# Performance work log

Hardware: AMD Instinct MI355X
Metric: run time of the kernel (lower is better)

Reference implementation:

```python
import jax, jax.numpy as jnp
import numpy as np

N_NODES = 100000
N_EDGES = 1600000
IN_F, HID_F, OUT_F = 128, 128, 128


def setup_inputs() -> dict:
    key = jax.random.key(0)
    ks = jax.random.split(key, 12)
    x = jax.random.normal(ks[0], (N_NODES, IN_F), dtype=jnp.float32)
    src = jax.random.randint(ks[1], (N_EDGES,), 0, N_NODES)
    dst = jax.random.randint(ks[2], (N_EDGES,), 0, N_NODES)
    s = 1.0 / np.sqrt(IN_F)
    W1_self = jax.random.uniform(ks[3], (HID_F, IN_F), minval=-s, maxval=s)
    W1_neigh = jax.random.uniform(ks[4], (HID_F, IN_F), minval=-s, maxval=s)
    b1 = jnp.zeros((HID_F,), jnp.float32)
    s2 = 1.0 / np.sqrt(HID_F)
    W2_self = jax.random.uniform(ks[5], (OUT_F, HID_F), minval=-s2, maxval=s2)
    W2_neigh = jax.random.uniform(ks[6], (OUT_F, HID_F), minval=-s2, maxval=s2)
    b2 = jnp.zeros((OUT_F,), jnp.float32)
    s3 = 1.0 / np.sqrt(OUT_F)
    W3 = jax.random.uniform(ks[7], (OUT_F, OUT_F), minval=-s3, maxval=s3)
    b3 = jax.random.uniform(ks[8], (OUT_F,), minval=-s3, maxval=s3)
    return {"x": x, "src": src, "dst": dst,
            "W1_self": W1_self, "W1_neigh": W1_neigh, "b1": b1,
            "W2_self": W2_self, "W2_neigh": W2_neigh, "b2": b2,
            "W3": W3, "b3": b3}


def _sage_conv(h, src, dst, W_self, W_neigh, b):
    # DGL SAGEConv 'mean': h_neigh = mean over in-neighbors (src -> dst)
    msg = h[src]  # [E, d] irregular gather
    summed = jax.ops.segment_sum(msg, dst, num_segments=N_NODES)  # [N, d]
    deg = jax.ops.segment_sum(jnp.ones((src.shape[0],), h.dtype), dst,
                              num_segments=N_NODES)
    h_neigh = summed / jnp.clip(deg, 1.0)[:, None]
    return h @ W_self.T + h_neigh @ W_neigh.T + b


def reference(x, src, dst, W1_self, W1_neigh, b1, W2_self, W2_neigh, b2, W3, b3):
    h = _sage_conv(x, src, dst, W1_self, W1_neigh, b1)
    h = jax.nn.relu(h)
    h = _sage_conv(h, src, dst, W2_self, W2_neigh, b2)
    return h @ W3.T + b3
```

## Files before the change

kernel.cpp:

```cpp
#include <hip/hip_runtime.h>

#define N_NODES 100000
#define N_EDGES 1600000
#define F 128
#define NB_SCAN ((N_NODES + 1023) / 1024)
#define NSUB 32
#define SUB_NODES (N_NODES / NSUB)
#define BCAP 128
#define PCAP 65536
#define NCVT ((N_NODES * F / 8 + 255) / 256)

typedef short short8 __attribute__((ext_vector_type(8)));
typedef float f32x4 __attribute__((ext_vector_type(4)));
typedef unsigned short ushort_t;
typedef ushort_t ushort8 __attribute__((ext_vector_type(8)));

__device__ __forceinline__ ushort_t f2b(float f) {
    union { float f; unsigned u; } v; v.f = f;
    unsigned r = v.u + 0x7fff + ((v.u >> 16) & 1);
    return (ushort_t)(r >> 16);
}


__global__ __launch_bounds__(256) void k_bucket(const int* __restrict__ src,
                                                const int* __restrict__ dst,
                                                int2* __restrict__ pairs,
                                                int* __restrict__ gcur) {
    __shared__ int2 lbuf[NSUB * BCAP];
    __shared__ int lcnt[NSUB], fbase[NSUB], fcnt[NSUB];
    const int tid = threadIdx.x;
    if (tid < NSUB) lcnt[tid] = 0;
    __syncthreads();

    for (int base = blockIdx.x * 1024; base < N_EDGES; base += gridDim.x * 1024) {
#pragma unroll
        for (int r = 0; r < 4; ++r) {
            int idx = base + r * 256 + tid;
            if (idx < N_EDGES) {
                int d = dst[idx], s = src[idx];
                int p = d / SUB_NODES;
                int dl = d - p * SUB_NODES;
                int slot = atomicAdd(&lcnt[p], 1);
                if (slot < BCAP) lbuf[p * BCAP + slot] = make_int2(dl, s);
                else {
                    int g = atomicAdd(&gcur[p], 1);
                    pairs[(size_t)p * PCAP + g] = make_int2(dl, s);
                }
            }
        }
        __syncthreads();
        if (tid < NSUB) {
            int c = lcnt[tid]; if (c > BCAP) c = BCAP;
            fcnt[tid] = c;
            fbase[tid] = atomicAdd(&gcur[tid], c);
        }
        __syncthreads();
        for (int p = 0; p < NSUB; ++p) {
            int c = fcnt[p];
            for (int i = tid; i < c; i += 256)
                pairs[(size_t)p * PCAP + fbase[p] + i] = lbuf[p * BCAP + i];
        }
        __syncthreads();
        if (tid < NSUB) lcnt[tid] = 0;
        __syncthreads();
    }
}

__global__ __launch_bounds__(1024) void k_histb(const int2* __restrict__ pairs,
                                                const int* __restrict__ gcur,
                                                int* __restrict__ cnt) {
    __shared__ int hc[SUB_NODES];
    const int p = blockIdx.x;
    for (int i = threadIdx.x; i < SUB_NODES; i += 1024) hc[i] = 0;
    __syncthreads();
    const int n = gcur[p];
    const int2* __restrict__ sl = pairs + (size_t)p * PCAP;
    for (int i = threadIdx.x; i < n; i += 1024) atomicAdd(&hc[sl[i].x], 1);
    __syncthreads();
    for (int i = threadIdx.x; i < SUB_NODES; i += 1024)
        cnt[p * SUB_NODES + i] = hc[i];
}

__global__ __launch_bounds__(1024) void k_scan1(const int* __restrict__ cnt,
                                                int* __restrict__ tmp,
                                                int* __restrict__ bsum) {
    __shared__ int ws[16];
    const int t = threadIdx.x, lane = t & 63, w = t >> 6;
    const int gid = blockIdx.x * 1024 + t;
    int v = (gid < N_NODES) ? cnt[gid] : 0;
    int x = v;
#pragma unroll
    for (int off = 1; off < 64; off <<= 1) {
        int y = __shfl_up(x, off, 64);
        if (lane >= off) x += y;
    }
    if (lane == 63) ws[w] = x;
    __syncthreads();
    if (w == 0) {
        int s = (lane < 16) ? ws[lane] : 0;
#pragma unroll
        for (int off = 1; off < 16; off <<= 1) {
            int y = __shfl_up(s, off, 64);
            if (lane >= off) s += y;
        }
        if (lane < 16) ws[lane] = s;
    }
    __syncthreads();
    int base = (w == 0) ? 0 : ws[w - 1];
    int incl = base + x;
    if (gid < N_NODES) tmp[gid] = incl;
    if (t == 1023) bsum[blockIdx.x] = incl;
}

__global__ __launch_bounds__(256) void k_scan23(const int* __restrict__ tmp,
                                                const int* __restrict__ bsum,
                                                int* __restrict__ row_ptr) {
    __shared__ int excl[NB_SCAN];
    const int t = threadIdx.x;
    if (t < 64) {
        const int lane = t;
        int v0 = (lane < NB_SCAN) ? bsum[lane] : 0;
        int v1 = (64 + lane < NB_SCAN) ? bsum[64 + lane] : 0;
        int x0 = v0;
#pragma unroll
        for (int off = 1; off < 64; off <<= 1) {
            int y = __shfl_up(x0, off, 64);
            if (lane >= off) x0 += y;
        }
        int tot0 = __shfl(x0, 63, 64);
        int x1 = v1;
#pragma unroll
        for (int off = 1; off < 64; off <<= 1) {
            int y = __shfl_up(x1, off, 64);
            if (lane >= off) x1 += y;
        }
        if (lane < NB_SCAN) excl[lane] = x0 - v0;
        if (64 + lane < NB_SCAN) excl[64 + lane] = tot0 + x1 - v1;
    }
    __syncthreads();
    int gid = blockIdx.x * 256 + t;
    if (gid >= N_NODES) return;
    row_ptr[gid + 1] = excl[gid >> 10] + tmp[gid];
    if (gid == 0) row_ptr[0] = 0;
}

__global__ __launch_bounds__(1024) void k_place(const int2* __restrict__ pairs,
                                                const int* __restrict__ gcur,
                                                const int* __restrict__ row_ptr,
                                                int* __restrict__ col) {
    __shared__ int cur[SUB_NODES];
    const int p = blockIdx.x;
    for (int i = threadIdx.x; i < SUB_NODES; i += 1024)
        cur[i] = row_ptr[p * SUB_NODES + i];
    __syncthreads();
    const int n = gcur[p];
    const int2* __restrict__ sl = pairs + (size_t)p * PCAP;
    for (int i = threadIdx.x; i < n; i += 1024) {
        int2 pr = sl[i];
        int pos = atomicAdd(&cur[pr.x], 1);
        col[pos] = pr.y;
    }
}

__global__ void k_prep(const float* __restrict__ x, ushort_t* __restrict__ xb,
                       const float* __restrict__ W1s, const float* __restrict__ W1n,
                       const float* __restrict__ W2s, const float* __restrict__ W2n,
                       const float* __restrict__ W3, const float* __restrict__ b2,
                       const float* __restrict__ b3,
                       ushort_t* __restrict__ wb, float* __restrict__ bc) {
    const int blk = blockIdx.x, t = threadIdx.x;
    if (blk < NCVT) {
        int i = blk * 256 + t;
        if (i >= N_NODES * F / 8) return;
        const float4* p = reinterpret_cast<const float4*>(x) + (size_t)i * 2;
        float4 a = p[0], b = p[1];
        ushort8 r;
        r[0] = f2b(a.x); r[1] = f2b(a.y); r[2] = f2b(a.z); r[3] = f2b(a.w);
        r[4] = f2b(b.x); r[5] = f2b(b.y); r[6] = f2b(b.z); r[7] = f2b(b.w);
        *reinterpret_cast<ushort8*>(xb + (size_t)i * 8) = r;
        return;
    }
    const int b = blk - NCVT;
    if (b < 128) {
        int g = b * 256 + t;
        float v = (g < F * F) ? W1s[g] : W1n[g - F * F];
        wb[g] = f2b(v);
    } else if (b < 256) {
        int g = (b - 128) * 256 + t;
        int m = g >> 14, rem = g & 16383, i = rem >> 7, j = rem & 127;
        const float* __restrict__ W2 = m ? W2n : W2s;
        float s = 0.f;
#pragma unroll 8
        for (int k = 0; k < F; ++k) s += W3[i * F + k] * W2[k * F + j];
        wb[2 * F * F + g] = f2b(s);
    } else if (t < F) {
        float s = b3[t];
#pragma unroll 8
        for (int k = 0; k < F; ++k) s += W3[t * F + k] * b2[k];
        bc[t] = s;
    }
}


__global__ __launch_bounds__(256) void k_agg(const ushort_t* __restrict__ h,
                                             const int* __restrict__ row_ptr,
                                             const int* __restrict__ col,
                                             ushort_t* __restrict__ out) {
    int node = (blockIdx.x * blockDim.x + threadIdx.x) >> 6;
    if (node >= N_NODES) return;
    const int lane = threadIdx.x & 63;
    const int loff = lane * 2;
    int beg = row_ptr[node], end = row_ptr[node + 1];
    float ax = 0.f, ay = 0.f;
    int e = beg;
    for (; e + 4 <= end; e += 4) {
        int s0 = __builtin_amdgcn_readfirstlane(col[e]);
        int s1 = __builtin_amdgcn_readfirstlane(col[e + 1]);
        int s2 = __builtin_amdgcn_readfirstlane(col[e + 2]);
        int s3 = __builtin_amdgcn_readfirstlane(col[e + 3]);
        unsigned v0 = *reinterpret_cast<const unsigned*>(h + ((size_t)s0 << 7) + loff);
        unsigned v1 = *reinterpret_cast<const unsigned*>(h + ((size_t)s1 << 7) + loff);
        unsigned v2 = *reinterpret_cast<const unsigned*>(h + ((size_t)s2 << 7) + loff);
        unsigned v3 = *reinterpret_cast<const unsigned*>(h + ((size_t)s3 << 7) + loff);
        ax += __uint_as_float(v0 << 16); ay += __uint_as_float(v0 & 0xffff0000u);
        ax += __uint_as_float(v1 << 16); ay += __uint_as_float(v1 & 0xffff0000u);
        ax += __uint_as_float(v2 << 16); ay += __uint_as_float(v2 & 0xffff0000u);
        ax += __uint_as_float(v3 << 16); ay += __uint_as_float(v3 & 0xffff0000u);
    }
    for (; e < end; ++e) {
        int s = __builtin_amdgcn_readfirstlane(col[e]);
        unsigned v = *reinterpret_cast<const unsigned*>(h + ((size_t)s << 7) + loff);
        ax += __uint_as_float(v << 16);
        ay += __uint_as_float(v & 0xffff0000u);
    }
    int deg = end - beg;
    float inv = 1.0f / (float)(deg > 0 ? deg : 1);
    unsigned r = ((unsigned)f2b(ax * inv)) | (((unsigned)f2b(ay * inv)) << 16);
    *reinterpret_cast<unsigned*>(out + (size_t)node * F + lane * 2) = r;
}


template <bool RELU, bool F32OUT>
__global__ __launch_bounds__(512) void k_layer(
        const ushort_t* __restrict__ A0, const ushort_t* __restrict__ A1,
        const ushort_t* __restrict__ W0, const ushort_t* __restrict__ W1,
        const float* __restrict__ bias, void* __restrict__ outv) {
    const int t = threadIdx.x;
    const int lane = t & 63;
    const int wid = t >> 6;
    const int wr = wid >> 2;
    const int wc = wid & 3;
    const int node0 = blockIdx.x * 128;
    const int arow = lane & 15;
    const int kgrp = lane >> 4;

    f32x4 acc[4][2];
#pragma unroll
    for (int fr = 0; fr < 4; ++fr)
#pragma unroll
        for (int fc = 0; fc < 2; ++fc) acc[fr][fc] = (f32x4)(0.f);

#pragma unroll
    for (int ph = 0; ph < 2; ++ph) {
        const ushort_t* __restrict__ A = ph ? A1 : A0;
        const ushort_t* __restrict__ W = ph ? W1 : W0;

        short8 bfrag[4][2];
#pragma unroll
        for (int ks = 0; ks < 4; ++ks)
#pragma unroll
            for (int fc = 0; fc < 2; ++fc) {
                int c = wc * 32 + fc * 16 + arow;
                bfrag[ks][fc] = *reinterpret_cast<const short8*>(W + c * F + ks * 32 + kgrp * 8);
            }

#pragma unroll
        for (int ks = 0; ks < 4; ++ks) {
            short8 afrag[4];
#pragma unroll
            for (int fr = 0; fr < 4; ++fr) {
                int r = node0 + wr * 64 + fr * 16 + arow;
                if (r > N_NODES - 1) r = N_NODES - 1;
                afrag[fr] = *reinterpret_cast<const short8*>(A + (size_t)r * F + ks * 32 + kgrp * 8);
            }
#pragma unroll
            for (int fr = 0; fr < 4; ++fr)
#pragma unroll
                for (int fc = 0; fc < 2; ++fc)
                    acc[fr][fc] = __builtin_amdgcn_mfma_f32_16x16x32_bf16(
                        afrag[fr], bfrag[ks][fc], acc[fr][fc], 0, 0, 0);
        }
    }

#pragma unroll
    for (int fr = 0; fr < 4; ++fr)
#pragma unroll
        for (int fc = 0; fc < 2; ++fc) {
            int c = wc * 32 + fc * 16 + (lane & 15);
            float bv = bias[c];
#pragma unroll
            for (int r4 = 0; r4 < 4; ++r4) {
                int row = node0 + wr * 64 + fr * 16 + (lane >> 4) * 4 + r4;
                if (row >= N_NODES) continue;
                float v = acc[fr][fc][r4] + bv;
                if (RELU) v = fmaxf(v, 0.f);
                if (F32OUT)
                    reinterpret_cast<float*>(outv)[(size_t)row * F + c] = v;
                else
                    reinterpret_cast<ushort_t*>(outv)[(size_t)row * F + c] = f2b(v);
            }
        }
}


extern "C" void kernel_launch(void* const* d_in, const int* in_sizes, int n_in,
                              void* d_out, int out_size, void* d_ws, size_t ws_size,
                              hipStream_t stream) {
    const float* x   = (const float*)d_in[0];
    const int*   src = (const int*)d_in[1];
    const int*   dst = (const int*)d_in[2];
    const float* W1s = (const float*)d_in[3];
    const float* W1n = (const float*)d_in[4];
    const float* b1  = (const float*)d_in[5];
    const float* W2s = (const float*)d_in[6];
    const float* W2n = (const float*)d_in[7];
    const float* b2  = (const float*)d_in[8];
    const float* W3  = (const float*)d_in[9];
    const float* b3  = (const float*)d_in[10];
    float* out = (float*)d_out;

    char* p = (char*)d_ws;
    auto align512 = [](size_t v) { return (v + 511) & ~(size_t)511; };
    int* row_ptr = (int*)p;        p += align512((N_NODES + 1) * sizeof(int));
    int* cnt     = (int*)p;        p += align512((size_t)N_NODES * sizeof(int));
    int* stmp    = (int*)p;        p += align512((size_t)N_NODES * sizeof(int));
    int* bsum    = (int*)p;        p += align512(256 * sizeof(int));
    int* gcur    = (int*)p;        p += align512(NSUB * sizeof(int));
    int* col     = (int*)p;        p += align512((size_t)N_EDGES * sizeof(int));
    ushort_t* wb = (ushort_t*)p;   p += align512((size_t)4 * F * F * sizeof(ushort_t));
    float* bc    = (float*)p;      p += align512(F * sizeof(float));
    ushort_t* xb = (ushort_t*)p;   p += align512((size_t)N_NODES * F * sizeof(ushort_t));
    ushort_t* aggb = (ushort_t*)p; p += align512((size_t)N_NODES * F * sizeof(ushort_t));
    ushort_t* h1b  = (ushort_t*)p; p += align512((size_t)N_NODES * F * sizeof(ushort_t));
    int2* pairs = (int2*)aggb;

    hipMemsetAsync(gcur, 0, NSUB * sizeof(int), stream);
    k_bucket<<<512, 256, 0, stream>>>(src, dst, pairs, gcur);
    k_histb<<<NSUB, 1024, 0, stream>>>(pairs, gcur, cnt);
    k_scan1<<<NB_SCAN, 1024, 0, stream>>>(cnt, stmp, bsum);
    k_scan23<<<(N_NODES + 255) / 256, 256, 0, stream>>>(stmp, bsum, row_ptr);
    k_place<<<NSUB, 1024, 0, stream>>>(pairs, gcur, row_ptr, col);

    k_prep<<<NCVT + 257, 256, 0, stream>>>(x, xb, W1s, W1n, W2s, W2n, W3, b2, b3, wb, bc);

    const int agg_grid = (N_NODES + 3) / 4;
    const int gemm_grid = (N_NODES + 127) / 128;

    k_agg<<<agg_grid, 256, 0, stream>>>(xb, row_ptr, col, aggb);
    k_layer<true, false><<<gemm_grid, 512, 0, stream>>>(
        xb, aggb, wb + 0 * F * F, wb + 1 * F * F, b1, h1b);

    k_agg<<<agg_grid, 256, 0, stream>>>(h1b, row_ptr, col, aggb);
    k_layer<false, true><<<gemm_grid, 512, 0, stream>>>(
        h1b, aggb, wb + 2 * F * F, wb + 3 * F * F, bc, out);
}
```

Baseline: 360.8 us.

## Fuse bucket and prep kernels; deepen gather unroll in aggregation

```diff
diff --git a/kernel.cpp b/kernel.cpp
--- a/kernel.cpp
+++ b/kernel.cpp
@@ -9,6 +9,8 @@
 #define BCAP 128
 #define PCAP 65536
 #define NCVT ((N_NODES * F / 8 + 255) / 256)
+#define BUCKET_BLOCKS 512
+#define PREP_BLOCKS (NCVT + 257)
 
 typedef short short8 __attribute__((ext_vector_type(8)));
 typedef float f32x4 __attribute__((ext_vector_type(4)));
@@ -22,17 +24,58 @@
 }
 
 
-__global__ __launch_bounds__(256) void k_bucket(const int* __restrict__ src,
-                                                const int* __restrict__ dst,
-                                                int2* __restrict__ pairs,
-                                                int* __restrict__ gcur) {
+__global__ __launch_bounds__(256) void k_bucket_prep(
+        const int* __restrict__ src, const int* __restrict__ dst,
+        int2* __restrict__ pairs, int* __restrict__ gcur,
+        const float* __restrict__ x, ushort_t* __restrict__ xb,
+        const float* __restrict__ W1s, const float* __restrict__ W1n,
+        const float* __restrict__ W2s, const float* __restrict__ W2n,
+        const float* __restrict__ W3, const float* __restrict__ b2,
+        const float* __restrict__ b3,
+        ushort_t* __restrict__ wb, float* __restrict__ bc) {
+    const int tid = threadIdx.x;
+
+    if (blockIdx.x >= BUCKET_BLOCKS) {
+        const int blk = blockIdx.x - BUCKET_BLOCKS;
+        if (blk < NCVT) {
+            int i = blk * 256 + tid;
+            if (i >= N_NODES * F / 8) return;
+            const float4* p = reinterpret_cast<const float4*>(x) + (size_t)i * 2;
+            float4 a = p[0], b = p[1];
+            ushort8 r;
+            r[0] = f2b(a.x); r[1] = f2b(a.y); r[2] = f2b(a.z); r[3] = f2b(a.w);
+            r[4] = f2b(b.x); r[5] = f2b(b.y); r[6] = f2b(b.z); r[7] = f2b(b.w);
+            *reinterpret_cast<ushort8*>(xb + (size_t)i * 8) = r;
+            return;
+        }
+        const int b = blk - NCVT;
+        if (b < 128) {
+            int g = b * 256 + tid;
+            float v = (g < F * F) ? W1s[g] : W1n[g - F * F];
+            wb[g] = f2b(v);
+        } else if (b < 256) {
+            int g = (b - 128) * 256 + tid;
+            int m = g >> 14, rem = g & 16383, i = rem >> 7, j = rem & 127;
+            const float* __restrict__ W2 = m ? W2n : W2s;
+            float s = 0.f;
+#pragma unroll 8
+            for (int k = 0; k < F; ++k) s += W3[i * F + k] * W2[k * F + j];
+            wb[2 * F * F + g] = f2b(s);
+        } else if (tid < F) {
+            float s = b3[tid];
+#pragma unroll 8
+            for (int k = 0; k < F; ++k) s += W3[tid * F + k] * b2[k];
+            bc[tid] = s;
+        }
+        return;
+    }
+
     __shared__ int2 lbuf[NSUB * BCAP];
     __shared__ int lcnt[NSUB], fbase[NSUB], fcnt[NSUB];
-    const int tid = threadIdx.x;
     if (tid < NSUB) lcnt[tid] = 0;
     __syncthreads();
 
-    for (int base = blockIdx.x * 1024; base < N_EDGES; base += gridDim.x * 1024) {
+    for (int base = blockIdx.x * 1024; base < N_EDGES; base += BUCKET_BLOCKS * 1024) {
 #pragma unroll
         for (int r = 0; r < 4; ++r) {
             int idx = base + r * 256 + tid;
@@ -162,45 +205,6 @@
     }
 }
 
-__global__ void k_prep(const float* __restrict__ x, ushort_t* __restrict__ xb,
-                       const float* __restrict__ W1s, const float* __restrict__ W1n,
-                       const float* __restrict__ W2s, const float* __restrict__ W2n,
-                       const float* __restrict__ W3, const float* __restrict__ b2,
-                       const float* __restrict__ b3,
-                       ushort_t* __restrict__ wb, float* __restrict__ bc) {
-    const int blk = blockIdx.x, t = threadIdx.x;
-    if (blk < NCVT) {
-        int i = blk * 256 + t;
-        if (i >= N_NODES * F / 8) return;
-        const float4* p = reinterpret_cast<const float4*>(x) + (size_t)i * 2;
-        float4 a = p[0], b = p[1];
-        ushort8 r;
-        r[0] = f2b(a.x); r[1] = f2b(a.y); r[2] = f2b(a.z); r[3] = f2b(a.w);
-        r[4] = f2b(b.x); r[5] = f2b(b.y); r[6] = f2b(b.z); r[7] = f2b(b.w);
-        *reinterpret_cast<ushort8*>(xb + (size_t)i * 8) = r;
-        return;
-    }
-    const int b = blk - NCVT;
-    if (b < 128) {
-        int g = b * 256 + t;
-        float v = (g < F * F) ? W1s[g] : W1n[g - F * F];
-        wb[g] = f2b(v);
-    } else if (b < 256) {
-        int g = (b - 128) * 256 + t;
-        int m = g >> 14, rem = g & 16383, i = rem >> 7, j = rem & 127;
-        const float* __restrict__ W2 = m ? W2n : W2s;
-        float s = 0.f;
-#pragma unroll 8
-        for (int k = 0; k < F; ++k) s += W3[i * F + k] * W2[k * F + j];
-        wb[2 * F * F + g] = f2b(s);
-    } else if (t < F) {
-        float s = b3[t];
-#pragma unroll 8
-        for (int k = 0; k < F; ++k) s += W3[t * F + k] * b2[k];
-        bc[t] = s;
-    }
-}
-
 
 __global__ __launch_bounds__(256) void k_agg(const ushort_t* __restrict__ h,
                                              const int* __restrict__ row_ptr,
@@ -209,34 +213,29 @@
     int node = (blockIdx.x * blockDim.x + threadIdx.x) >> 6;
     if (node >= N_NODES) return;
     const int lane = threadIdx.x & 63;
-    const int loff = lane * 2;
-    int beg = row_ptr[node], end = row_ptr[node + 1];
+    const unsigned loff = (unsigned)lane * 4u;
+    const char* __restrict__ hb = reinterpret_cast<const char*>(h);
+    const int beg = row_ptr[node], end = row_ptr[node + 1];
     float ax = 0.f, ay = 0.f;
-    int e = beg;
-    for (; e + 4 <= end; e += 4) {
-        int s0 = __builtin_amdgcn_readfirstlane(col[e]);
-        int s1 = __builtin_amdgcn_readfirstlane(col[e + 1]);
-        int s2 = __builtin_amdgcn_readfirstlane(col[e + 2]);
-        int s3 = __builtin_amdgcn_readfirstlane(col[e + 3]);
-        unsigned v0 = *reinterpret_cast<const unsigned*>(h + ((size_t)s0 << 7) + loff);
-        unsigned v1 = *reinterpret_cast<const unsigned*>(h + ((size_t)s1 << 7) + loff);
-        unsigned v2 = *reinterpret_cast<const unsigned*>(h + ((size_t)s2 << 7) + loff);
-        unsigned v3 = *reinterpret_cast<const unsigned*>(h + ((size_t)s3 << 7) + loff);
-        ax += __uint_as_float(v0 << 16); ay += __uint_as_float(v0 & 0xffff0000u);
-        ax += __uint_as_float(v1 << 16); ay += __uint_as_float(v1 & 0xffff0000u);
-        ax += __uint_as_float(v2 << 16); ay += __uint_as_float(v2 & 0xffff0000u);
-        ax += __uint_as_float(v3 << 16); ay += __uint_as_float(v3 & 0xffff0000u);
-    }
-    for (; e < end; ++e) {
-        int s = __builtin_amdgcn_readfirstlane(col[e]);
-        unsigned v = *reinterpret_cast<const unsigned*>(h + ((size_t)s << 7) + loff);
-        ax += __uint_as_float(v << 16);
-        ay += __uint_as_float(v & 0xffff0000u);
+    for (int e = beg; e < end; e += 8) {
+        unsigned v[8];
+#pragma unroll
+        for (int u = 0; u < 8; ++u) {
+            int idx = e + u; idx = (idx < end) ? idx : end - 1;
+            unsigned s = (unsigned)col[idx];
+            v[u] = *reinterpret_cast<const unsigned*>(hb + (size_t)((s << 8) + loff));
+        }
+#pragma unroll
+        for (int u = 0; u < 8; ++u) {
+            unsigned vv = (e + u < end) ? v[u] : 0u;
+            ax += __uint_as_float(vv << 16);
+            ay += __uint_as_float(vv & 0xffff0000u);
+        }
     }
     int deg = end - beg;
     float inv = 1.0f / (float)(deg > 0 ? deg : 1);
     unsigned r = ((unsigned)f2b(ax * inv)) | (((unsigned)f2b(ay * inv)) << 16);
-    *reinterpret_cast<unsigned*>(out + (size_t)node * F + lane * 2) = r;
+    *reinterpret_cast<unsigned*>(out + ((size_t)node << 7) + lane * 2) = r;
 }
 
 
@@ -345,14 +344,13 @@
     int2* pairs = (int2*)aggb;
 
     hipMemsetAsync(gcur, 0, NSUB * sizeof(int), stream);
-    k_bucket<<<512, 256, 0, stream>>>(src, dst, pairs, gcur);
+    k_bucket_prep<<<BUCKET_BLOCKS + PREP_BLOCKS, 256, 0, stream>>>(
+        src, dst, pairs, gcur, x, xb, W1s, W1n, W2s, W2n, W3, b2, b3, wb, bc);
     k_histb<<<NSUB, 1024, 0, stream>>>(pairs, gcur, cnt);
     k_scan1<<<NB_SCAN, 1024, 0, stream>>>(cnt, stmp, bsum);
     k_scan23<<<(N_NODES + 255) / 256, 256, 0, stream>>>(stmp, bsum, row_ptr);
     k_place<<<NSUB, 1024, 0, stream>>>(pairs, gcur, row_ptr, col);
 
-    k_prep<<<NCVT + 257, 256, 0, stream>>>(x, xb, W1s, W1n, W2s, W2n, W3, b2, b3, wb, bc);
-
     const int agg_grid = (N_NODES + 3) / 4;
     const int gemm_grid = (N_NODES + 127) / 128;
 
```

New measurement: 324.8 us. 1.11x faster.
